# Kernel tuning notes

Hardware: AMD Instinct MI355X
Metric: run time of the kernel (lower is better)

Reference implementation:

```python
import jax, jax.numpy as jnp
import numpy as np

N, E = 100000, 800000
IN, HID, H, C, L, OUT = 32, 128, 4, 32, 3, 5
NEG_SLOPE = 0.2
EPS = 1e-5


def setup_inputs() -> dict:
    key = jax.random.key(0)
    ks = jax.random.split(key, 20)
    s = 0.1
    inp = {
        "x": jax.random.normal(ks[0], (N, IN), jnp.float32),
        "edge_index": jax.random.randint(ks[1], (2, E), 0, N, jnp.int64),
        "edge_attr": jax.random.uniform(ks[2], (E, 1), jnp.float32),
        "Win": jax.random.normal(ks[3], (IN, HID), jnp.float32) * s,
        "b_in": jnp.zeros((HID,), jnp.float32),
        "Wg": jax.random.normal(ks[4], (L, HID, H * C), jnp.float32) * s,
        "bg": jnp.zeros((L, H * C), jnp.float32),
        "a_src": jax.random.normal(ks[5], (L, H, C), jnp.float32) * s,
        "a_dst": jax.random.normal(ks[6], (L, H, C), jnp.float32) * s,
        "We": jax.random.normal(ks[7], (L, 1, H * C), jnp.float32) * s,
        "a_edge": jax.random.normal(ks[8], (L, H, C), jnp.float32) * s,
        "ln_w": jnp.ones((L, HID), jnp.float32),
        "ln_b": jnp.zeros((L, HID), jnp.float32),
        "Wout": jax.random.normal(ks[9], (HID, OUT), jnp.float32) * s,
        "bout": jnp.zeros((OUT,), jnp.float32),
    }
    return inp


def _add_self_loops(src, dst, ea):
    # PyG fill_value='mean': self-loop attr = mean of incoming edge attrs per node
    ones = jnp.ones((src.shape[0],), ea.dtype)
    deg = jax.ops.segment_sum(ones, dst, N)
    loop_attr = jax.ops.segment_sum(ea, dst, N) / jnp.maximum(deg, 1.0)[:, None]
    idx = jnp.arange(N, dtype=src.dtype)
    return (jnp.concatenate([src, idx]), jnp.concatenate([dst, idx]),
            jnp.concatenate([ea, loop_attr], axis=0))


def _gat_conv(x, src, dst, ea, Wg, bg, a_s, a_d, We, a_e):
    xh = (x @ Wg).reshape(N, H, C)                    # [N,H,C]
    al_s = jnp.einsum('nhc,hc->nh', xh, a_s)          # [N,H]
    al_d = jnp.einsum('nhc,hc->nh', xh, a_d)
    ee = (ea @ We).reshape(-1, H, C)                  # [Et,H,C]
    al_e = jnp.einsum('ehc,hc->eh', ee, a_e)
    logits = jax.nn.leaky_relu(al_s[src] + al_d[dst] + al_e, NEG_SLOPE)
    m = jax.ops.segment_max(logits, dst, N)
    m = jnp.where(jnp.isfinite(m), m, 0.0)
    ex = jnp.exp(logits - m[dst])
    den = jax.ops.segment_sum(ex, dst, N)
    alpha = ex / (den[dst] + 1e-16)                   # segment softmax over dst
    out = jax.ops.segment_sum(alpha[:, :, None] * xh[src], dst, N)
    return out.reshape(N, H * C) + bg


def _graph_layernorm(h, w, b):
    # PyG LayerNorm(mode='graph'): normalize over all nodes and features
    h = h - jnp.mean(h)
    var = jnp.mean(h * h)
    return h / jnp.sqrt(var + EPS) * w + b


def reference(x, edge_index, edge_attr, Win, b_in, Wg, bg, a_src, a_dst, We,
              a_edge, ln_w, ln_b, Wout, bout):
    src, dst = edge_index[0], edge_index[1]
    src, dst, ea = _add_self_loops(src, dst, edge_attr)
    h = x @ Win + b_in
    for l in range(L):
        g = _gat_conv(h, src, dst, ea, Wg[l], bg[l], a_src[l], a_dst[l],
                      We[l], a_edge[l])
        g = _graph_layernorm(g, ln_w[l], ln_b[l])
        h = jax.nn.relu(g + h)
    return h @ Wout + bout
```

## Files before the change

### kernel.cpp

```cpp
#include <hip/hip_runtime.h>
#include <hip/hip_bf16.h>

#define NN 100000
#define EE 800000
#define HID 128
#define NH 4
#define CH 32
#define NL 3
#define NOUT 5
#define NEG_SLOPE 0.2f
#define LN_EPS 1e-5f
#define GCAP 64
#define NB_SCAN 98
#define HQ (HID / 2)
#define WB_LSZ 9216
#define HB4 782
#define SB4 782
#define NG64 1563

typedef unsigned int u32;
typedef __attribute__((ext_vector_type(8))) short bf16x8;
typedef __attribute__((ext_vector_type(4))) float f32x4;

static __device__ __forceinline__ float bflo(u32 r) { return __uint_as_float(r << 16); }
static __device__ __forceinline__ float bfhi(u32 r) { return __uint_as_float(r & 0xffff0000u); }
static __device__ __forceinline__ unsigned short f2bf(float x) {
    union U { __hip_bfloat16 b; unsigned short s; } u;
    u.b = __float2bfloat16(x);
    return u.s;
}
static __device__ __forceinline__ u32 pack2(float a, float b) {
    return (u32)f2bf(a) | ((u32)f2bf(b) << 16);
}
static __device__ __forceinline__ float lrelu(float x) {
    return x > 0.f ? x : NEG_SLOPE * x;
}

__global__ void hist_prep_kernel(const int* __restrict__ ei, int* __restrict__ cnt,
                                 u32* __restrict__ slot,
                                 const float* __restrict__ We, const float* __restrict__ a_e,
                                 float* __restrict__ wedot,
                                 const float* __restrict__ Win, const float* __restrict__ b_in,
                                 const float* __restrict__ Wg, float* __restrict__ wf,
                                 const float* __restrict__ a_src, const float* __restrict__ a_dst,
                                 u32* __restrict__ wb, float* __restrict__ wga) {
    int b = blockIdx.x, t = threadIdx.x;
    if (b < HB4) {
        int e0 = b * 1024 + t;
        #pragma unroll
        for (int k = 0; k < 4; k++) {
            int e = e0 + k * 256;
            if (e < EE) {
                int d = ei[EE + e];
                int s = atomicAdd(&cnt[d], 1);
                slot[e] = ((u32)d << 8) | (u32)s;
            }
        }
        return;
    }
    if (b == HB4) {
        if (t < NL * NH) {
            int l = t >> 2, hh = t & 3;
            float s = 0.f;
            #pragma unroll
            for (int c = 0; c < CH; c++)
                s += We[l * HID + hh * CH + c] * a_e[l * HID + hh * CH + c];
            wedot[t] = s;
        }
        for (int i = t; i < HID * 8; i += 256) {
            int m = i >> 3, j = i & 7;
            int hh = j & 3;
            const float* a = (j < 4) ? (a_src + hh * CH) : (a_dst + hh * CH);
            const float* wrow = Wg + (size_t)m * HID + hh * CH;
            float s = 0.f;
            #pragma unroll
            for (int c = 0; c < CH; c++) s += wrow[c] * a[c];
            wga[i] = s;
        }
        return;
    }
    if (b < HB4 + 18) {
        int idx = (b - HB4 - 1) * 256 + t;
        if (idx >= 33 * HID) return;
        int r = idx >> 7, c = idx & 127;
        float acc = 0.f;
        for (int k = 0; k < HID; k++) {
            float a = (r < 32) ? Win[r * HID + k] : b_in[k];
            acc += a * Wg[(size_t)k * HID + c];
        }
        wf[r * HID + c] = acc;
        return;
    }
    {
        int idx = (b - HB4 - 18) * 256 + t;
        if (idx >= 2 * 2304) return;
        int l = idx / 2304;
        int rem = idx % 2304;
        int ks = rem / 576;
        int ct = (rem % 576) / 64;
        int lane = rem % 64;
        int q = lane >> 4, n = lane & 15;
        const float* W = Wg + (size_t)(l + 1) * HID * HID;
        float v[8];
        if (ct < 8) {
            #pragma unroll
            for (int j = 0; j < 8; j++) {
                int k = ks * 32 + q * 8 + j;
                v[j] = W[(size_t)k * HID + ct * 16 + n];
            }
        } else {
            #pragma unroll
            for (int j = 0; j < 8; j++) v[j] = 0.f;
            if (n < 8) {
                const float* a = (n < 4) ? (a_src + (l + 1) * HID + (n & 3) * CH)
                                         : (a_dst + (l + 1) * HID + (n & 3) * CH);
                #pragma unroll
                for (int j = 0; j < 8; j++) {
                    int k = ks * 32 + q * 8 + j;
                    const float* wrow = W + (size_t)k * HID + (n & 3) * CH;
                    float s = 0.f;
                    for (int c = 0; c < CH; c++) s += wrow[c] * a[c];
                    v[j] = s;
                }
            }
        }
        u32* dst = wb + (size_t)l * WB_LSZ + (size_t)((ks * 9 + ct) * 64 + lane) * 4;
        dst[0] = pack2(v[0], v[1]); dst[1] = pack2(v[2], v[3]);
        dst[2] = pack2(v[4], v[5]); dst[3] = pack2(v[6], v[7]);
    }
}

__global__ __launch_bounds__(1024) void scan_prep2_kernel(const int* __restrict__ cnt,
        int* __restrict__ rowptr, int* __restrict__ sums, int* __restrict__ prefixes,
        int* __restrict__ flags,
        const float* __restrict__ Win, const float* __restrict__ b_in,
        const float* __restrict__ wga, float* __restrict__ wf, u32* __restrict__ wb2) {
    if (blockIdx.x >= NB_SCAN) {
        int b = blockIdx.x - NB_SCAN;
        int lane = threadIdx.x;
        if (lane >= 64) return;
        int q = lane >> 4, n = lane & 15;
        if (b == 17) {
            if (lane < 8) {
                float s = 0.f;
                for (int m = 0; m < HID; m++) s += b_in[m] * wga[m * 8 + lane];
                wf[33 * HID + lane] = s;
            }
            return;
        }
        float v[8];
        if (b < 8) {
            #pragma unroll
            for (int j = 0; j < 8; j++) v[j] = Win[(q * 8 + j) * HID + b * 16 + n];
        } else if (b < 16) {
            int ct = b - 8;
            #pragma unroll
            for (int j = 0; j < 8; j++) v[j] = wf[(q * 8 + j) * HID + ct * 16 + n];
        } else {
            #pragma unroll
            for (int j = 0; j < 8; j++) v[j] = 0.f;
            if (n < 8) {
                #pragma unroll
                for (int j = 0; j < 8; j++) {
                    const float* wrow = Win + (q * 8 + j) * HID;
                    float s = 0.f;
                    for (int m = 0; m < HID; m++) s += wrow[m] * wga[m * 8 + n];
                    v[j] = s;
                }
            }
        }
        u32* dst = wb2 + (size_t)(b * 64 + lane) * 4;
        dst[0] = pack2(v[0], v[1]); dst[1] = pack2(v[2], v[3]);
        dst[2] = pack2(v[4], v[5]); dst[3] = pack2(v[6], v[7]);
        return;
    }
    __shared__ int ws[16];
    __shared__ int bprefix;
    int b = blockIdx.x;
    int gid = b * 1024 + threadIdx.x;
    int v = (gid < NN) ? cnt[gid] : 0;
    int lane = threadIdx.x & 63, wid = threadIdx.x >> 6;
    int s = v;
    #pragma unroll
    for (int off = 1; off < 64; off <<= 1) {
        int t2 = __shfl_up(s, off, 64);
        if (lane >= off) s += t2;
    }
    if (lane == 63) ws[wid] = s;
    __syncthreads();
    int add = 0;
    for (int w2 = 0; w2 < wid; w2++) add += ws[w2];
    int incl = s + add;
    if (threadIdx.x == 0) {
        int total = 0;
        for (int w2 = 0; w2 < 16; w2++) total += ws[w2];
        atomicExch(&sums[b], total);
        __threadfence();
        atomicExch(&flags[b], 1);
        int pfx = 0;
        for (int i = b - 1; i >= 0; i--) {
            int f;
            do { f = atomicAdd(&flags[i], 0); } while (f == 0);
            if (f == 2) { pfx += atomicAdd(&prefixes[i], 0); break; }
            pfx += atomicAdd(&sums[i], 0);
        }
        atomicExch(&prefixes[b], pfx + total);
        __threadfence();
        atomicExch(&flags[b], 2);
        bprefix = pfx;
    }
    __syncthreads();
    int pfx = bprefix;
    if (gid <= NN) rowptr[gid] = pfx + incl - v;
}

__global__ __launch_bounds__(256) void scatter_ingemm_kernel(
        const int* __restrict__ ei, const float* __restrict__ ea,
        const int* __restrict__ rowptr, const u32* __restrict__ slot,
        uint2* __restrict__ edges,
        const float* __restrict__ x, const u32* __restrict__ wb2,
        const float* __restrict__ wf, const float* __restrict__ b_in,
        u32* __restrict__ h, u32* __restrict__ xh,
        float* __restrict__ al_s, float* __restrict__ al_d) {
    __shared__ u32 xsu[1024];
    if (blockIdx.x < SB4) {
        int e0 = blockIdx.x * 1024 + threadIdx.x;
        #pragma unroll
        for (int k = 0; k < 4; k++) {
            int e = e0 + k * 256;
            if (e < EE) {
                u32 p = slot[e];
                int d = (int)(p >> 8);
                int pos = rowptr[d] + (int)(p & 255u);
                edges[pos] = make_uint2((u32)ei[e], __float_as_uint(ea[e]));
            }
        }
        return;
    }
    int t = threadIdx.x;
    int wv = t >> 6, lane = t & 63;
    int q = lane >> 4, n16 = lane & 15;
    int n0 = (blockIdx.x - SB4) * 64;
    {
        int row = t >> 2, qq = t & 3;
        int gr = n0 + row;
        int rt = row >> 4, m = row & 15;
        uint4 op = make_uint4(0u, 0u, 0u, 0u);
        if (gr < NN) {
            float4 vA = *(const float4*)&x[(size_t)gr * 32 + qq * 8];
            float4 vB = *(const float4*)&x[(size_t)gr * 32 + qq * 8 + 4];
            op.x = pack2(vA.x, vA.y); op.y = pack2(vA.z, vA.w);
            op.z = pack2(vB.x, vB.y); op.w = pack2(vB.z, vB.w);
        }
        *(uint4*)&xsu[(rt * 64 + qq * 16 + m) * 4] = op;
    }
    bf16x8 bwin[2], bwf[2], bal;
    #pragma unroll
    for (int cc = 0; cc < 2; cc++) {
        uint4 r0 = *(const uint4*)&wb2[(size_t)(((wv * 2 + cc)) * 64 + lane) * 4];
        uint4 r1 = *(const uint4*)&wb2[(size_t)((8 + wv * 2 + cc) * 64 + lane) * 4];
        bwin[cc] = __builtin_bit_cast(bf16x8, r0);
        bwf[cc]  = __builtin_bit_cast(bf16x8, r1);
    }
    {
        uint4 r = *(const uint4*)&wb2[(size_t)(16 * 64 + lane) * 4];
        bal = __builtin_bit_cast(bf16x8, r);
    }
    __syncthreads();
    f32x4 acch[4][2], accx[4][2], accal[4];
    #pragma unroll
    for (int rt = 0; rt < 4; rt++) {
        acch[rt][0] = (f32x4){0.f, 0.f, 0.f, 0.f};
        acch[rt][1] = (f32x4){0.f, 0.f, 0.f, 0.f};
        accx[rt][0] = (f32x4){0.f, 0.f, 0.f, 0.f};
        accx[rt][1] = (f32x4){0.f, 0.f, 0.f, 0.f};
        accal[rt]   = (f32x4){0.f, 0.f, 0.f, 0.f};
    }
    #pragma unroll
    for (int rt = 0; rt < 4; rt++) {
        uint4 araw = *(const uint4*)&xsu[(rt * 64 + lane) * 4];
        bf16x8 af = __builtin_bit_cast(bf16x8, araw);
        acch[rt][0] = __builtin_amdgcn_mfma_f32_16x16x32_bf16(af, bwin[0], acch[rt][0], 0, 0, 0);
        acch[rt][1] = __builtin_amdgcn_mfma_f32_16x16x32_bf16(af, bwin[1], acch[rt][1], 0, 0, 0);
        accx[rt][0] = __builtin_amdgcn_mfma_f32_16x16x32_bf16(af, bwf[0], accx[rt][0], 0, 0, 0);
        accx[rt][1] = __builtin_amdgcn_mfma_f32_16x16x32_bf16(af, bwf[1], accx[rt][1], 0, 0, 0);
        if (wv == 3)
            accal[rt] = __builtin_amdgcn_mfma_f32_16x16x32_bf16(af, bal, accal[rt], 0, 0, 0);
    }
    float bi[2], bfv[2];
    #pragma unroll
    for (int cc = 0; cc < 2; cc++) {
        int col = (wv * 2 + cc) * 16 + n16;
        bi[cc] = b_in[col];
        bfv[cc] = wf[32 * HID + col];
    }
    float bfa = (wv == 3 && n16 < 8) ? wf[33 * HID + n16] : 0.f;
    #pragma unroll
    for (int rt = 0; rt < 4; rt++) {
        #pragma unroll
        for (int reg = 0; reg < 4; reg++) {
            int row = n0 + rt * 16 + q * 4 + reg;
            #pragma unroll
            for (int cc = 0; cc < 2; cc++) {
                float v = acch[rt][cc][reg] + bi[cc];
                float vp = __shfl_xor(v, 1, 64);
                float u = accx[rt][cc][reg] + bfv[cc];
                float up = __shfl_xor(u, 1, 64);
                if (!(n16 & 1) && row < NN) {
                    int colp = (wv * 2 + cc) * 8 + (n16 >> 1);
                    h[(size_t)row * HQ + colp] = pack2(v, vp);
                    xh[(size_t)row * HQ + colp] = pack2(u, up);
                }
            }
            if (wv == 3 && row < NN && n16 < 8) {
                float v = accal[rt][reg] + bfa;
                if (n16 < 4) al_s[row * 4 + n16] = v;
                else         al_d[row * 4 + (n16 - 4)] = v;
            }
        }
    }
}

__global__ __launch_bounds__(256) void gemm_mfma_kernel(const u32* __restrict__ h,
        const u32* __restrict__ wb, u32* __restrict__ xh, const u32* __restrict__ g,
        const float* __restrict__ lnw, const float* __restrict__ lnb,
        const float* __restrict__ partials, u32* __restrict__ hout,
        float* __restrict__ al_s, float* __restrict__ al_d) {
    __shared__ u32 hsu[4096];
    __shared__ float sred[8];
    int n0 = blockIdx.x * 64;
    int t = threadIdx.x;
    int wv = t >> 6, lane = t & 63;
    int q = lane >> 4, n16 = lane & 15;

    {
        const float4* pp = (const float4*)partials;
        float4 v0 = pp[t * 2], v1 = pp[t * 2 + 1];
        float s = v0.x + v0.z + v1.x + v1.z;
        float qq = v0.y + v0.w + v1.y + v1.w;
        #pragma unroll
        for (int off = 1; off <= 32; off <<= 1) {
            s += __shfl_xor(s, off, 64);
            qq += __shfl_xor(qq, off, 64);
        }
        if (lane == 0) { sred[wv * 2] = s; sred[wv * 2 + 1] = qq; }
    }
    __syncthreads();
    float S = sred[0] + sred[2] + sred[4] + sred[6];
    float Q = sred[1] + sred[3] + sred[5] + sred[7];
    const float M = (float)NN * (float)HID;
    float mean = S / M;
    float rstd = rsqrtf(fmaxf(Q / M - mean * mean, 0.f) + LN_EPS);

    bf16x8 bfrag[2][4];
    #pragma unroll
    for (int ks = 0; ks < 4; ks++) {
        #pragma unroll
        for (int cc = 0; cc < 2; cc++) {
            int ct = wv * 2 + cc;
            uint4 r = *(const uint4*)&wb[(size_t)((ks * 9 + ct) * 64 + lane) * 4];
            bfrag[cc][ks] = __builtin_bit_cast(bf16x8, r);
        }
    }
    bf16x8 bal[4];
    #pragma unroll
    for (int ks = 0; ks < 4; ks++) {
        uint4 r = *(const uint4*)&wb[(size_t)((ks * 9 + 8) * 64 + lane) * 4];
        bal[ks] = __builtin_bit_cast(bf16x8, r);
    }

    {
        int row = t >> 2;
        int qq = t & 3;
        int gr = n0 + row;
        int rt = row >> 4, m = row & 15;
        #pragma unroll
        for (int ks = 0; ks < 4; ks++) {
            int kk = ks * 32 + qq * 8;
            uint4 op = make_uint4(0u, 0u, 0u, 0u);
            if (gr < NN) {
                size_t base = (size_t)gr * HQ + (kk >> 1);
                uint4 gp = *(const uint4*)&g[base];
                uint4 hp = *(const uint4*)&h[base];
                float4 wA = *(const float4*)&lnw[kk];
                float4 wB = *(const float4*)&lnw[kk + 4];
                float4 bA = *(const float4*)&lnb[kk];
                float4 bB = *(const float4*)&lnb[kk + 4];
                float v0 = fmaxf((bflo(gp.x) - mean) * rstd * wA.x + bA.x + bflo(hp.x), 0.f);
                float v1 = fmaxf((bfhi(gp.x) - mean) * rstd * wA.y + bA.y + bfhi(hp.x), 0.f);
                float v2 = fmaxf((bflo(gp.y) - mean) * rstd * wA.z + bA.z + bflo(hp.y), 0.f);
                float v3 = fmaxf((bfhi(gp.y) - mean) * rstd * wA.w + bA.w + bfhi(hp.y), 0.f);
                float v4 = fmaxf((bflo(gp.z) - mean) * rstd * wB.x + bB.x + bflo(hp.z), 0.f);
                float v5 = fmaxf((bfhi(gp.z) - mean) * rstd * wB.y + bB.y + bfhi(hp.z), 0.f);
                float v6 = fmaxf((bflo(gp.w) - mean) * rstd * wB.z + bB.z + bflo(hp.w), 0.f);
                float v7 = fmaxf((bfhi(gp.w) - mean) * rstd * wB.w + bB.w + bfhi(hp.w), 0.f);
                op.x = pack2(v0, v1); op.y = pack2(v2, v3);
                op.z = pack2(v4, v5); op.w = pack2(v6, v7);
                *(uint4*)&hout[base] = op;
            }
            *(uint4*)&hsu[((rt * 4 + ks) * 64 + qq * 16 + m) * 4] = op;
        }
    }
    __syncthreads();

    f32x4 acc[4][2];
    f32x4 accal[4];
    #pragma unroll
    for (int rt = 0; rt < 4; rt++) {
        acc[rt][0] = (f32x4){0.f, 0.f, 0.f, 0.f};
        acc[rt][1] = (f32x4){0.f, 0.f, 0.f, 0.f};
        accal[rt]  = (f32x4){0.f, 0.f, 0.f, 0.f};
    }
    #pragma unroll
    for (int rt = 0; rt < 4; rt++) {
        #pragma unroll
        for (int ks = 0; ks < 4; ks++) {
            uint4 araw = *(const uint4*)&hsu[((rt * 4 + ks) * 64 + lane) * 4];
            bf16x8 af = __builtin_bit_cast(bf16x8, araw);
            acc[rt][0] = __builtin_amdgcn_mfma_f32_16x16x32_bf16(af, bfrag[0][ks], acc[rt][0], 0, 0, 0);
            acc[rt][1] = __builtin_amdgcn_mfma_f32_16x16x32_bf16(af, bfrag[1][ks], acc[rt][1], 0, 0, 0);
            if (wv == 3)
                accal[rt] = __builtin_amdgcn_mfma_f32_16x16x32_bf16(af, bal[ks], accal[rt], 0, 0, 0);
        }
    }

    #pragma unroll
    for (int rt = 0; rt < 4; rt++) {
        #pragma unroll
        for (int reg = 0; reg < 4; reg++) {
            int row = n0 + rt * 16 + q * 4 + reg;
            #pragma unroll
            for (int cc = 0; cc < 2; cc++) {
                float v = acc[rt][cc][reg];
                float vp = __shfl_xor(v, 1, 64);
                if (!(n16 & 1) && row < NN) {
                    int colp = (wv * 2 + cc) * 8 + (n16 >> 1);
                    xh[(size_t)row * HQ + colp] = pack2(v, vp);
                }
            }
            if (wv == 3 && row < NN && n16 < 8) {
                float v = accal[rt][reg];
                if (n16 < 4) al_s[row * 4 + n16] = v;
                else         al_d[row * 4 + (n16 - 4)] = v;
            }
        }
    }
}

__global__ __launch_bounds__(256) void gat_agg_kernel(const int* __restrict__ rowptr,
        const uint2* __restrict__ edges, const u32* __restrict__ xh,
        const float* __restrict__ al_s, const float* __restrict__ al_d,
        const float* __restrict__ wedot, const float* __restrict__ bg,
        u32* __restrict__ g, float* __restrict__ partials) {
    __shared__ float lds_ex[4][GCAP * 4];
    __shared__ float lds_ea[4][GCAP];
    __shared__ int lds_src[4][GCAP];
    int wv = threadIdx.x >> 6, lane = threadIdx.x & 63;
    int base = (blockIdx.x * 4 + wv) * 4;
    if (base >= NN) return;
    float* ex_w = lds_ex[wv];
    float* ea_w = lds_ea[wv];
    int* src_w = lds_src[wv];
    int b1 = base + 1 < NN ? base + 1 : NN;
    int b2 = base + 2 < NN ? base + 2 : NN;
    int b3 = base + 3 < NN ? base + 3 : NN;
    int b4 = base + 4 < NN ? base + 4 : NN;
    int r0 = rowptr[base], r1 = rowptr[b1], r2 = rowptr[b2], r3 = rowptr[b3], r4 = rowptr[b4];
    int span = r4 - r0;
    int ncached = span < GCAP ? span : GCAP;
    float wd0 = wedot[0], wd1 = wedot[1], wd2 = wedot[2], wd3 = wedot[3];

    for (int i = lane; i < ncached; i += 64) {
        int gi = r0 + i;
        uint2 e = edges[gi];
        int s = (int)e.x;
        float eav = __uint_as_float(e.y);
        int d = (gi >= r1) + (gi >= r2) + (gi >= r3);
        float4 aldv = *(const float4*)&al_d[(base + d) * 4];
        float4 als = *(const float4*)&al_s[s * 4];
        float e0 = __expf(lrelu(als.x + aldv.x + eav * wd0));
        float e1 = __expf(lrelu(als.y + aldv.y + eav * wd1));
        float e2 = __expf(lrelu(als.z + aldv.z + eav * wd2));
        float e3 = __expf(lrelu(als.w + aldv.w + eav * wd3));
        src_w[i] = s;
        ea_w[i] = eav;
        *(float4*)&ex_w[i * 4] = make_float4(e0, e1, e2, e3);
    }

    int nl = lane >> 4, cg = lane & 15;
    int n = base + nl;
    bool nvalid = n < NN;
    int ls = (nl == 0 ? r0 : nl == 1 ? r1 : nl == 2 ? r2 : r3) - r0;
    int le = (nl == 0 ? r1 : nl == 1 ? r2 : nl == 2 ? r3 : r4) - r0;
    int lec = le < ncached ? le : ncached;
    int head = cg >> 2;
    int c4 = cg * 4;
    float wdh = head == 0 ? wd0 : head == 1 ? wd1 : head == 2 ? wd2 : wd3;
    float a0 = 0.f, a1 = 0.f, a2 = 0.f, a3 = 0.f;
    float a4 = 0.f, a5 = 0.f, a6 = 0.f, a7 = 0.f, den = 0.f, easum = 0.f;
    int j = ls;
    for (; j + 3 < lec; j += 4) {
        int s0 = src_w[j], s1 = src_w[j + 1], s2 = src_w[j + 2], s3 = src_w[j + 3];
        float e0 = ex_w[j * 4 + head],       e1 = ex_w[(j + 1) * 4 + head];
        float e2 = ex_w[(j + 2) * 4 + head], e3 = ex_w[(j + 3) * 4 + head];
        uint4 x0 = *(const uint4*)&xh[(size_t)s0 * HQ + c4];
        uint4 x1 = *(const uint4*)&xh[(size_t)s1 * HQ + c4];
        uint4 x2 = *(const uint4*)&xh[(size_t)s2 * HQ + c4];
        uint4 x3 = *(const uint4*)&xh[(size_t)s3 * HQ + c4];
        den += e0 + e1 + e2 + e3;
        easum += ea_w[j] + ea_w[j + 1] + ea_w[j + 2] + ea_w[j + 3];
        a0 += e0 * bflo(x0.x); a1 += e0 * bfhi(x0.x);
        a2 += e0 * bflo(x0.y); a3 += e0 * bfhi(x0.y);
        a4 += e0 * bflo(x0.z); a5 += e0 * bfhi(x0.z);
        a6 += e0 * bflo(x0.w); a7 += e0 * bfhi(x0.w);
        a0 += e1 * bflo(x1.x); a1 += e1 * bfhi(x1.x);
        a2 += e1 * bflo(x1.y); a3 += e1 * bfhi(x1.y);
        a4 += e1 * bflo(x1.z); a5 += e1 * bfhi(x1.z);
        a6 += e1 * bflo(x1.w); a7 += e1 * bfhi(x1.w);
        a0 += e2 * bflo(x2.x); a1 += e2 * bfhi(x2.x);
        a2 += e2 * bflo(x2.y); a3 += e2 * bfhi(x2.y);
        a4 += e2 * bflo(x2.z); a5 += e2 * bfhi(x2.z);
        a6 += e2 * bflo(x2.w); a7 += e2 * bfhi(x2.w);
        a0 += e3 * bflo(x3.x); a1 += e3 * bfhi(x3.x);
        a2 += e3 * bflo(x3.y); a3 += e3 * bfhi(x3.y);
        a4 += e3 * bflo(x3.z); a5 += e3 * bfhi(x3.z);
        a6 += e3 * bflo(x3.w); a7 += e3 * bfhi(x3.w);
    }
    for (; j < lec; j++) {
        int s0 = src_w[j];
        float e0 = ex_w[j * 4 + head];
        uint4 x0 = *(const uint4*)&xh[(size_t)s0 * HQ + c4];
        den += e0;
        easum += ea_w[j];
        a0 += e0 * bflo(x0.x); a1 += e0 * bfhi(x0.x);
        a2 += e0 * bflo(x0.y); a3 += e0 * bfhi(x0.y);
        a4 += e0 * bflo(x0.z); a5 += e0 * bfhi(x0.z);
        a6 += e0 * bflo(x0.w); a7 += e0 * bfhi(x0.w);
    }
    if (le > lec && nvalid) {
        float aldh = al_d[n * 4 + head];
        for (int jt = (ls > lec ? ls : lec); jt < le; jt++) {
            uint2 e = edges[r0 + jt];
            int s = (int)e.x;
            float eav = __uint_as_float(e.y);
            float ex = __expf(lrelu(al_s[s * 4 + head] + aldh + eav * wdh));
            den += ex;
            easum += eav;
            uint4 x0 = *(const uint4*)&xh[(size_t)s * HQ + c4];
            a0 += ex * bflo(x0.x); a1 += ex * bfhi(x0.x);
            a2 += ex * bflo(x0.y); a3 += ex * bfhi(x0.y);
            a4 += ex * bflo(x0.z); a5 += ex * bfhi(x0.z);
            a6 += ex * bflo(x0.w); a7 += ex * bfhi(x0.w);
        }
    }
    if (nvalid) {
        float mea = easum / fmaxf((float)(le - ls), 1.0f);
        float alh = al_s[n * 4 + head] + al_d[n * 4 + head];
        float ex = __expf(lrelu(alh + mea * wdh));
        den += ex;
        uint4 x0 = *(const uint4*)&xh[(size_t)n * HQ + c4];
        a0 += ex * bflo(x0.x); a1 += ex * bfhi(x0.x);
        a2 += ex * bflo(x0.y); a3 += ex * bfhi(x0.y);
        a4 += ex * bflo(x0.z); a5 += ex * bfhi(x0.z);
        a6 += ex * bflo(x0.w); a7 += ex * bfhi(x0.w);
    }

    float inv = 1.0f / (den + 1e-16f);
    int c0 = cg * 8;
    float4 bgA = *(const float4*)&bg[c0];
    float4 bgB = *(const float4*)&bg[c0 + 4];
    float o0 = a0 * inv + bgA.x, o1 = a1 * inv + bgA.y;
    float o2 = a2 * inv + bgA.z, o3 = a3 * inv + bgA.w;
    float o4 = a4 * inv + bgB.x, o5 = a5 * inv + bgB.y;
    float o6 = a6 * inv + bgB.z, o7 = a7 * inv + bgB.w;
    float ss = 0.f, sq = 0.f;
    if (nvalid) {
        uint4 op;
        op.x = pack2(o0, o1); op.y = pack2(o2, o3);
        op.z = pack2(o4, o5); op.w = pack2(o6, o7);
        *(uint4*)&g[(size_t)n * HQ + c4] = op;
        ss = o0 + o1 + o2 + o3 + o4 + o5 + o6 + o7;
        sq = o0 * o0 + o1 * o1 + o2 * o2 + o3 * o3
           + o4 * o4 + o5 * o5 + o6 * o6 + o7 * o7;
    }
    #pragma unroll
    for (int off = 1; off <= 32; off <<= 1) {
        ss += __shfl_xor(ss, off, 64);
        sq += __shfl_xor(sq, off, 64);
    }
    if (lane == 0) {
        int sl = ((blockIdx.x * 4 + wv) & 1023) * 2;
        atomicAdd(&partials[sl], ss);
        atomicAdd(&partials[sl + 1], sq);
    }
}

__global__ __launch_bounds__(256) void ln_out_kernel(const u32* __restrict__ g,
        const u32* __restrict__ h, const float* __restrict__ lnw,
        const float* __restrict__ lnb, const float* __restrict__ partials,
        const float* __restrict__ Wout, const float* __restrict__ bout,
        float* __restrict__ out) {
    __shared__ float wsh[HID * NOUT];
    __shared__ float sred[8];
    int t = threadIdx.x;
    int wv = t >> 6, lane = t & 63;
    {
        const float4* pp = (const float4*)partials;
        float4 v0 = pp[t * 2], v1 = pp[t * 2 + 1];
        float s = v0.x + v0.z + v1.x + v1.z;
        float qq = v0.y + v0.w + v1.y + v1.w;
        #pragma unroll
        for (int off = 1; off <= 32; off <<= 1) {
            s += __shfl_xor(s, off, 64);
            qq += __shfl_xor(qq, off, 64);
        }
        if (lane == 0) { sred[wv * 2] = s; sred[wv * 2 + 1] = qq; }
    }
    for (int i = t; i < HID * NOUT; i += 256) wsh[i] = Wout[i];
    __syncthreads();
    float S = sred[0] + sred[2] + sred[4] + sred[6];
    float Q = sred[1] + sred[3] + sred[5] + sred[7];
    const float M = (float)NN * (float)HID;
    float mean = S / M;
    float rstd = rsqrtf(fmaxf(Q / M - mean * mean, 0.f) + LN_EPS);

    int nl = lane >> 4, cg = lane & 15;
    int n = (blockIdx.x * 4 + wv) * 4 + nl;
    bool nvalid = n < NN;
    float p[NOUT] = {};
    if (nvalid) {
        int c0 = cg * 8;
        uint4 gv = *(const uint4*)&g[(size_t)n * HQ + cg * 4];
        uint4 hv = *(const uint4*)&h[(size_t)n * HQ + cg * 4];
        float4 wA = *(const float4*)&lnw[c0], wB = *(const float4*)&lnw[c0 + 4];
        float4 bA = *(const float4*)&lnb[c0], bB = *(const float4*)&lnb[c0 + 4];
        float o[8];
        o[0] = fmaxf((bflo(gv.x) - mean) * rstd * wA.x + bA.x + bflo(hv.x), 0.f);
        o[1] = fmaxf((bfhi(gv.x) - mean) * rstd * wA.y + bA.y + bfhi(hv.x), 0.f);
        o[2] = fmaxf((bflo(gv.y) - mean) * rstd * wA.z + bA.z + bflo(hv.y), 0.f);
        o[3] = fmaxf((bfhi(gv.y) - mean) * rstd * wA.w + bA.w + bfhi(hv.y), 0.f);
        o[4] = fmaxf((bflo(gv.z) - mean) * rstd * wB.x + bB.x + bflo(hv.z), 0.f);
        o[5] = fmaxf((bfhi(gv.z) - mean) * rstd * wB.y + bB.y + bfhi(hv.z), 0.f);
        o[6] = fmaxf((bflo(gv.w) - mean) * rstd * wB.z + bB.z + bflo(hv.w), 0.f);
        o[7] = fmaxf((bfhi(gv.w) - mean) * rstd * wB.w + bB.w + bfhi(hv.w), 0.f);
        #pragma unroll
        for (int jj = 0; jj < NOUT; jj++) {
            float acc = 0.f;
            #pragma unroll
            for (int k = 0; k < 8; k++) acc += o[k] * wsh[(c0 + k) * NOUT + jj];
            p[jj] = acc;
        }
    }
    #pragma unroll
    for (int off = 1; off <= 8; off <<= 1) {
        #pragma unroll
        for (int jj = 0; jj < NOUT; jj++) p[jj] += __shfl_xor(p[jj], off, 64);
    }
    if (cg == 0 && nvalid) {
        #pragma unroll
        for (int jj = 0; jj < NOUT; jj++)
            out[(size_t)n * NOUT + jj] = p[jj] + bout[jj];
    }
}

extern "C" void kernel_launch(void* const* d_in, const int* in_sizes, int n_in,
                              void* d_out, int out_size, void* d_ws, size_t ws_size,
                              hipStream_t stream) {
    const float* x      = (const float*)d_in[0];
    const int*   ei     = (const int*)d_in[1];
    const float* ea     = (const float*)d_in[2];
    const float* Win    = (const float*)d_in[3];
    const float* b_in   = (const float*)d_in[4];
    const float* Wg     = (const float*)d_in[5];
    const float* bg     = (const float*)d_in[6];
    const float* a_src  = (const float*)d_in[7];
    const float* a_dst  = (const float*)d_in[8];
    const float* We     = (const float*)d_in[9];
    const float* a_edge = (const float*)d_in[10];
    const float* ln_w   = (const float*)d_in[11];
    const float* ln_b   = (const float*)d_in[12];
    const float* Wout   = (const float*)d_in[13];
    const float* bout   = (const float*)d_in[14];
    float* out = (float*)d_out;

    char* w = (char*)d_ws;
    size_t off = 0;
    auto alloc = [&](size_t bytes) -> void* {
        void* p = w + off;
        off = (off + bytes + 255) & ~(size_t)255;
        return p;
    };
    int*   cnt      = (int*)alloc(NN * sizeof(int));
    float* partials = (float*)alloc(3 * 2048 * sizeof(float));
    int*   sums     = (int*)alloc(NB_SCAN * sizeof(int));
    int*   prefixes = (int*)alloc(NB_SCAN * sizeof(int));
    int*   flags    = (int*)alloc(NB_SCAN * sizeof(int));
    size_t zero_span = off;
    u32*   slot    = (u32*)alloc((size_t)EE * sizeof(u32));
    int*   rowptr  = (int*)alloc((NN + 1) * sizeof(int));
    uint2* edges   = (uint2*)alloc((size_t)EE * sizeof(uint2));
    u32*   h       = (u32*)alloc((size_t)NN * HQ * sizeof(u32));
    u32*   g       = (u32*)alloc((size_t)NN * HQ * sizeof(u32));
    u32*   xh      = (u32*)alloc((size_t)NN * HQ * sizeof(u32));
    float* al_s    = (float*)alloc((size_t)NN * NH * sizeof(float));
    float* al_d    = (float*)alloc((size_t)NN * NH * sizeof(float));
    float* wedot   = (float*)alloc(16 * sizeof(float));
    float* wf      = (float*)alloc(34 * HID * sizeof(float));
    float* wga     = (float*)alloc(HID * 8 * sizeof(float));
    u32*   wb      = (u32*)alloc((size_t)2 * WB_LSZ * sizeof(u32));
    u32*   wb2     = (u32*)alloc(17 * 64 * 4 * sizeof(u32));
    (void)ws_size; (void)n_in; (void)in_sizes; (void)out_size;

    hipMemsetAsync(d_ws, 0, zero_span, stream);
    hist_prep_kernel<<<HB4 + 36, 256, 0, stream>>>(ei, cnt, slot, We, a_edge, wedot,
                                                   Win, b_in, Wg, wf, a_src, a_dst,
                                                   wb, wga);
    scan_prep2_kernel<<<NB_SCAN + 18, 1024, 0, stream>>>(cnt, rowptr, sums, prefixes,
                                                         flags, Win, b_in, wga, wf, wb2);
    scatter_ingemm_kernel<<<SB4 + NG64, 256, 0, stream>>>(ei, ea, rowptr, slot, edges,
                                                          x, wb2, wf, b_in, h, xh,
                                                          al_s, al_d);
    for (int l = 0; l < NL; l++) {
        if (l > 0) {
            gemm_mfma_kernel<<<NG64, 256, 0, stream>>>(
                h, wb + (size_t)(l - 1) * WB_LSZ, xh, g,
                ln_w + (size_t)(l - 1) * HID, ln_b + (size_t)(l - 1) * HID,
                partials + (size_t)(l - 1) * 2048, h, al_s, al_d);
        }
        gat_agg_kernel<<<(NN + 15) / 16, 256, 0, stream>>>(
            rowptr, edges, xh, al_s, al_d, wedot + l * 4,
            bg + (size_t)l * HID, g, partials + (size_t)l * 2048);
    }

    ln_out_kernel<<<(NN + 15) / 16, 256, 0, stream>>>(g, h, ln_w + (size_t)2 * HID,
                                                      ln_b + (size_t)2 * HID,
                                                      partials + 2 * 2048, Wout, bout, out);
}
```

Baseline: 390.0 us.

## Process eight nodes per wavefront in GAT aggregation with 16 channels per lane

The GAT aggregation kernel now assigns eight destination nodes per wavefront instead of four, with each lane handling 16 channels (two 16-byte loads per neighbor row) rather than 8. It fetches the row pointers with one lane-parallel load plus shuffles and doubles the LDS edge cache to 128 entries. The histogram and scatter phases also process eight edges per thread with half as many blocks. This amortizes per-wave setup and edge-logit computation over more nodes, but it halves the number of waves and raises register pressure from the 16 accumulators, which may reduce occupancy and the memory-level parallelism of the gathers.

```diff
diff --git a/kernel.cpp b/kernel.cpp
--- a/kernel.cpp
+++ b/kernel.cpp
@@ -10,12 +10,12 @@
 #define NOUT 5
 #define NEG_SLOPE 0.2f
 #define LN_EPS 1e-5f
-#define GCAP 64
+#define GCAP 128
 #define NB_SCAN 98
 #define HQ (HID / 2)
 #define WB_LSZ 9216
-#define HB4 782
-#define SB4 782
+#define HB8 391
+#define SB8 391
 #define NG64 1563
 
 typedef unsigned int u32;
@@ -45,10 +45,10 @@
                                  const float* __restrict__ a_src, const float* __restrict__ a_dst,
                                  u32* __restrict__ wb, float* __restrict__ wga) {
     int b = blockIdx.x, t = threadIdx.x;
-    if (b < HB4) {
-        int e0 = b * 1024 + t;
-        #pragma unroll
-        for (int k = 0; k < 4; k++) {
+    if (b < HB8) {
+        int e0 = b * 2048 + t;
+        #pragma unroll
+        for (int k = 0; k < 8; k++) {
             int e = e0 + k * 256;
             if (e < EE) {
                 int d = ei[EE + e];
@@ -58,7 +58,7 @@
         }
         return;
     }
-    if (b == HB4) {
+    if (b == HB8) {
         if (t < NL * NH) {
             int l = t >> 2, hh = t & 3;
             float s = 0.f;
@@ -79,8 +79,8 @@
         }
         return;
     }
-    if (b < HB4 + 18) {
-        int idx = (b - HB4 - 1) * 256 + t;
+    if (b < HB8 + 18) {
+        int idx = (b - HB8 - 1) * 256 + t;
         if (idx >= 33 * HID) return;
         int r = idx >> 7, c = idx & 127;
         float acc = 0.f;
@@ -92,7 +92,7 @@
         return;
     }
     {
-        int idx = (b - HB4 - 18) * 256 + t;
+        int idx = (b - HB8 - 18) * 256 + t;
         if (idx >= 2 * 2304) return;
         int l = idx / 2304;
         int rem = idx % 2304;
@@ -223,10 +223,10 @@
         u32* __restrict__ h, u32* __restrict__ xh,
         float* __restrict__ al_s, float* __restrict__ al_d) {
     __shared__ u32 xsu[1024];
-    if (blockIdx.x < SB4) {
-        int e0 = blockIdx.x * 1024 + threadIdx.x;
-        #pragma unroll
-        for (int k = 0; k < 4; k++) {
+    if (blockIdx.x < SB8) {
+        int e0 = blockIdx.x * 2048 + threadIdx.x;
+        #pragma unroll
+        for (int k = 0; k < 8; k++) {
             int e = e0 + k * 256;
             if (e < EE) {
                 u32 p = slot[e];
@@ -240,7 +240,7 @@
     int t = threadIdx.x;
     int wv = t >> 6, lane = t & 63;
     int q = lane >> 4, n16 = lane & 15;
-    int n0 = (blockIdx.x - SB4) * 64;
+    int n0 = (blockIdx.x - SB8) * 64;
     {
         int row = t >> 2, qq = t & 3;
         int gr = n0 + row;
@@ -456,17 +456,20 @@
     __shared__ float lds_ea[4][GCAP];
     __shared__ int lds_src[4][GCAP];
     int wv = threadIdx.x >> 6, lane = threadIdx.x & 63;
-    int base = (blockIdx.x * 4 + wv) * 4;
+    int base = (blockIdx.x * 4 + wv) * 8;
     if (base >= NN) return;
     float* ex_w = lds_ex[wv];
     float* ea_w = lds_ea[wv];
     int* src_w = lds_src[wv];
-    int b1 = base + 1 < NN ? base + 1 : NN;
-    int b2 = base + 2 < NN ? base + 2 : NN;
-    int b3 = base + 3 < NN ? base + 3 : NN;
-    int b4 = base + 4 < NN ? base + 4 : NN;
-    int r0 = rowptr[base], r1 = rowptr[b1], r2 = rowptr[b2], r3 = rowptr[b3], r4 = rowptr[b4];
-    int span = r4 - r0;
+    int rv = 0;
+    if (lane < 9) {
+        int idx = base + lane;
+        rv = rowptr[idx < NN ? idx : NN];
+    }
+    int r0 = __shfl(rv, 0, 64), r1 = __shfl(rv, 1, 64), r2 = __shfl(rv, 2, 64);
+    int r3 = __shfl(rv, 3, 64), r4 = __shfl(rv, 4, 64), r5 = __shfl(rv, 5, 64);
+    int r6 = __shfl(rv, 6, 64), r7 = __shfl(rv, 7, 64), r8 = __shfl(rv, 8, 64);
+    int span = r8 - r0;
     int ncached = span < GCAP ? span : GCAP;
     float wd0 = wedot[0], wd1 = wedot[1], wd2 = wedot[2], wd3 = wedot[3];
 
@@ -475,7 +478,8 @@
         uint2 e = edges[gi];
         int s = (int)e.x;
         float eav = __uint_as_float(e.y);
-        int d = (gi >= r1) + (gi >= r2) + (gi >= r3);
+        int d = (gi >= r1) + (gi >= r2) + (gi >= r3) + (gi >= r4)
+              + (gi >= r5) + (gi >= r6) + (gi >= r7);
         float4 aldv = *(const float4*)&al_d[(base + d) * 4];
         float4 als = *(const float4*)&al_s[s * 4];
         float e0 = __expf(lrelu(als.x + aldv.x + eav * wd0));
@@ -487,101 +491,137 @@
         *(float4*)&ex_w[i * 4] = make_float4(e0, e1, e2, e3);
     }
 
-    int nl = lane >> 4, cg = lane & 15;
+    int nl = lane >> 3, cg = lane & 7;
     int n = base + nl;
     bool nvalid = n < NN;
-    int ls = (nl == 0 ? r0 : nl == 1 ? r1 : nl == 2 ? r2 : r3) - r0;
-    int le = (nl == 0 ? r1 : nl == 1 ? r2 : nl == 2 ? r3 : r4) - r0;
-    int lec = le < ncached ? le : ncached;
-    int head = cg >> 2;
-    int c4 = cg * 4;
+    int lsv, lev;
+    {
+        int ra = nl == 0 ? r0 : nl == 1 ? r1 : nl == 2 ? r2 : nl == 3 ? r3
+               : nl == 4 ? r4 : nl == 5 ? r5 : nl == 6 ? r6 : r7;
+        int rb = nl == 0 ? r1 : nl == 1 ? r2 : nl == 2 ? r3 : nl == 3 ? r4
+               : nl == 4 ? r5 : nl == 5 ? r6 : nl == 6 ? r7 : r8;
+        lsv = ra - r0; lev = rb - r0;
+    }
+    int lec = lev < ncached ? lev : ncached;
+    int head = cg >> 1;
+    int c8 = cg * 8;
     float wdh = head == 0 ? wd0 : head == 1 ? wd1 : head == 2 ? wd2 : wd3;
     float a0 = 0.f, a1 = 0.f, a2 = 0.f, a3 = 0.f;
-    float a4 = 0.f, a5 = 0.f, a6 = 0.f, a7 = 0.f, den = 0.f, easum = 0.f;
-    int j = ls;
-    for (; j + 3 < lec; j += 4) {
-        int s0 = src_w[j], s1 = src_w[j + 1], s2 = src_w[j + 2], s3 = src_w[j + 3];
-        float e0 = ex_w[j * 4 + head],       e1 = ex_w[(j + 1) * 4 + head];
-        float e2 = ex_w[(j + 2) * 4 + head], e3 = ex_w[(j + 3) * 4 + head];
-        uint4 x0 = *(const uint4*)&xh[(size_t)s0 * HQ + c4];
-        uint4 x1 = *(const uint4*)&xh[(size_t)s1 * HQ + c4];
-        uint4 x2 = *(const uint4*)&xh[(size_t)s2 * HQ + c4];
-        uint4 x3 = *(const uint4*)&xh[(size_t)s3 * HQ + c4];
-        den += e0 + e1 + e2 + e3;
-        easum += ea_w[j] + ea_w[j + 1] + ea_w[j + 2] + ea_w[j + 3];
-        a0 += e0 * bflo(x0.x); a1 += e0 * bfhi(x0.x);
-        a2 += e0 * bflo(x0.y); a3 += e0 * bfhi(x0.y);
-        a4 += e0 * bflo(x0.z); a5 += e0 * bfhi(x0.z);
-        a6 += e0 * bflo(x0.w); a7 += e0 * bfhi(x0.w);
-        a0 += e1 * bflo(x1.x); a1 += e1 * bfhi(x1.x);
-        a2 += e1 * bflo(x1.y); a3 += e1 * bfhi(x1.y);
-        a4 += e1 * bflo(x1.z); a5 += e1 * bfhi(x1.z);
-        a6 += e1 * bflo(x1.w); a7 += e1 * bfhi(x1.w);
-        a0 += e2 * bflo(x2.x); a1 += e2 * bfhi(x2.x);
-        a2 += e2 * bflo(x2.y); a3 += e2 * bfhi(x2.y);
-        a4 += e2 * bflo(x2.z); a5 += e2 * bfhi(x2.z);
-        a6 += e2 * bflo(x2.w); a7 += e2 * bfhi(x2.w);
-        a0 += e3 * bflo(x3.x); a1 += e3 * bfhi(x3.x);
-        a2 += e3 * bflo(x3.y); a3 += e3 * bfhi(x3.y);
-        a4 += e3 * bflo(x3.z); a5 += e3 * bfhi(x3.z);
-        a6 += e3 * bflo(x3.w); a7 += e3 * bfhi(x3.w);
-    }
-    for (; j < lec; j++) {
+    float a4 = 0.f, a5 = 0.f, a6 = 0.f, a7 = 0.f;
+    float a8 = 0.f, a9 = 0.f, aA = 0.f, aB = 0.f;
+    float aC = 0.f, aD = 0.f, aE = 0.f, aF = 0.f;
+    float den = 0.f, easum = 0.f;
+    int j = lsv;
+    for (; j + 1 < lec; j += 2) {
+        int s0 = src_w[j], s1 = src_w[j + 1];
+        float e0 = ex_w[j * 4 + head], e1 = ex_w[(j + 1) * 4 + head];
+        const u32* p0 = &xh[(size_t)s0 * HQ + c8];
+        const u32* p1 = &xh[(size_t)s1 * HQ + c8];
+        uint4 x0a = *(const uint4*)p0, x0b = *(const uint4*)(p0 + 4);
+        uint4 x1a = *(const uint4*)p1, x1b = *(const uint4*)(p1 + 4);
+        den += e0 + e1;
+        easum += ea_w[j] + ea_w[j + 1];
+        a0 += e0 * bflo(x0a.x); a1 += e0 * bfhi(x0a.x);
+        a2 += e0 * bflo(x0a.y); a3 += e0 * bfhi(x0a.y);
+        a4 += e0 * bflo(x0a.z); a5 += e0 * bfhi(x0a.z);
+        a6 += e0 * bflo(x0a.w); a7 += e0 * bfhi(x0a.w);
+        a8 += e0 * bflo(x0b.x); a9 += e0 * bfhi(x0b.x);
+        aA += e0 * bflo(x0b.y); aB += e0 * bfhi(x0b.y);
+        aC += e0 * bflo(x0b.z); aD += e0 * bfhi(x0b.z);
+        aE += e0 * bflo(x0b.w); aF += e0 * bfhi(x0b.w);
+        a0 += e1 * bflo(x1a.x); a1 += e1 * bfhi(x1a.x);
+        a2 += e1 * bflo(x1a.y); a3 += e1 * bfhi(x1a.y);
+        a4 += e1 * bflo(x1a.z); a5 += e1 * bfhi(x1a.z);
+        a6 += e1 * bflo(x1a.w); a7 += e1 * bfhi(x1a.w);
+        a8 += e1 * bflo(x1b.x); a9 += e1 * bfhi(x1b.x);
+        aA += e1 * bflo(x1b.y); aB += e1 * bfhi(x1b.y);
+        aC += e1 * bflo(x1b.z); aD += e1 * bfhi(x1b.z);
+        aE += e1 * bflo(x1b.w); aF += e1 * bfhi(x1b.w);
+    }
+    if (j < lec) {
         int s0 = src_w[j];
         float e0 = ex_w[j * 4 + head];
-        uint4 x0 = *(const uint4*)&xh[(size_t)s0 * HQ + c4];
+        const u32* p0 = &xh[(size_t)s0 * HQ + c8];
+        uint4 x0a = *(const uint4*)p0, x0b = *(const uint4*)(p0 + 4);
         den += e0;
         easum += ea_w[j];
-        a0 += e0 * bflo(x0.x); a1 += e0 * bfhi(x0.x);
-        a2 += e0 * bflo(x0.y); a3 += e0 * bfhi(x0.y);
-        a4 += e0 * bflo(x0.z); a5 += e0 * bfhi(x0.z);
-        a6 += e0 * bflo(x0.w); a7 += e0 * bfhi(x0.w);
-    }
-    if (le > lec && nvalid) {
+        a0 += e0 * bflo(x0a.x); a1 += e0 * bfhi(x0a.x);
+        a2 += e0 * bflo(x0a.y); a3 += e0 * bfhi(x0a.y);
+        a4 += e0 * bflo(x0a.z); a5 += e0 * bfhi(x0a.z);
+        a6 += e0 * bflo(x0a.w); a7 += e0 * bfhi(x0a.w);
+        a8 += e0 * bflo(x0b.x); a9 += e0 * bfhi(x0b.x);
+        aA += e0 * bflo(x0b.y); aB += e0 * bfhi(x0b.y);
+        aC += e0 * bflo(x0b.z); aD += e0 * bfhi(x0b.z);
+        aE += e0 * bflo(x0b.w); aF += e0 * bfhi(x0b.w);
+        j++;
+    }
+    if (lev > lec && nvalid) {
         float aldh = al_d[n * 4 + head];
-        for (int jt = (ls > lec ? ls : lec); jt < le; jt++) {
+        for (int jt = (lsv > lec ? lsv : lec); jt < lev; jt++) {
             uint2 e = edges[r0 + jt];
             int s = (int)e.x;
             float eav = __uint_as_float(e.y);
             float ex = __expf(lrelu(al_s[s * 4 + head] + aldh + eav * wdh));
             den += ex;
             easum += eav;
-            uint4 x0 = *(const uint4*)&xh[(size_t)s * HQ + c4];
-            a0 += ex * bflo(x0.x); a1 += ex * bfhi(x0.x);
-            a2 += ex * bflo(x0.y); a3 += ex * bfhi(x0.y);
-            a4 += ex * bflo(x0.z); a5 += ex * bfhi(x0.z);
-            a6 += ex * bflo(x0.w); a7 += ex * bfhi(x0.w);
+            const u32* p0 = &xh[(size_t)s * HQ + c8];
+            uint4 x0a = *(const uint4*)p0, x0b = *(const uint4*)(p0 + 4);
+            a0 += ex * bflo(x0a.x); a1 += ex * bfhi(x0a.x);
+            a2 += ex * bflo(x0a.y); a3 += ex * bfhi(x0a.y);
+            a4 += ex * bflo(x0a.z); a5 += ex * bfhi(x0a.z);
+            a6 += ex * bflo(x0a.w); a7 += ex * bfhi(x0a.w);
+            a8 += ex * bflo(x0b.x); a9 += ex * bfhi(x0b.x);
+            aA += ex * bflo(x0b.y); aB += ex * bfhi(x0b.y);
+            aC += ex * bflo(x0b.z); aD += ex * bfhi(x0b.z);
+            aE += ex * bflo(x0b.w); aF += ex * bfhi(x0b.w);
         }
     }
     if (nvalid) {
-        float mea = easum / fmaxf((float)(le - ls), 1.0f);
+        float mea = easum / fmaxf((float)(lev - lsv), 1.0f);
         float alh = al_s[n * 4 + head] + al_d[n * 4 + head];
         float ex = __expf(lrelu(alh + mea * wdh));
         den += ex;
-        uint4 x0 = *(const uint4*)&xh[(size_t)n * HQ + c4];
-        a0 += ex * bflo(x0.x); a1 += ex * bfhi(x0.x);
-        a2 += ex * bflo(x0.y); a3 += ex * bfhi(x0.y);
-        a4 += ex * bflo(x0.z); a5 += ex * bfhi(x0.z);
-        a6 += ex * bflo(x0.w); a7 += ex * bfhi(x0.w);
+        const u32* p0 = &xh[(size_t)n * HQ + c8];
+        uint4 x0a = *(const uint4*)p0, x0b = *(const uint4*)(p0 + 4);
+        a0 += ex * bflo(x0a.x); a1 += ex * bfhi(x0a.x);
+        a2 += ex * bflo(x0a.y); a3 += ex * bfhi(x0a.y);
+        a4 += ex * bflo(x0a.z); a5 += ex * bfhi(x0a.z);
+        a6 += ex * bflo(x0a.w); a7 += ex * bfhi(x0a.w);
+        a8 += ex * bflo(x0b.x); a9 += ex * bfhi(x0b.x);
+        aA += ex * bflo(x0b.y); aB += ex * bfhi(x0b.y);
+        aC += ex * bflo(x0b.z); aD += ex * bfhi(x0b.z);
+        aE += ex * bflo(x0b.w); aF += ex * bfhi(x0b.w);
     }
 
     float inv = 1.0f / (den + 1e-16f);
-    int c0 = cg * 8;
-    float4 bgA = *(const float4*)&bg[c0];
-    float4 bgB = *(const float4*)&bg[c0 + 4];
-    float o0 = a0 * inv + bgA.x, o1 = a1 * inv + bgA.y;
-    float o2 = a2 * inv + bgA.z, o3 = a3 * inv + bgA.w;
-    float o4 = a4 * inv + bgB.x, o5 = a5 * inv + bgB.y;
-    float o6 = a6 * inv + bgB.z, o7 = a7 * inv + bgB.w;
+    int c0 = cg * 16;
+    float4 bg0 = *(const float4*)&bg[c0];
+    float4 bg1 = *(const float4*)&bg[c0 + 4];
+    float4 bg2 = *(const float4*)&bg[c0 + 8];
+    float4 bg3 = *(const float4*)&bg[c0 + 12];
+    float o0 = a0 * inv + bg0.x, o1 = a1 * inv + bg0.y;
+    float o2 = a2 * inv + bg0.z, o3 = a3 * inv + bg0.w;
+    float o4 = a4 * inv + bg1.x, o5 = a5 * inv + bg1.y;
+    float o6 = a6 * inv + bg1.z, o7 = a7 * inv + bg1.w;
+    float o8 = a8 * inv + bg2.x, o9 = a9 * inv + bg2.y;
+    float oA = aA * inv + bg2.z, oB = aB * inv + bg2.w;
+    float oC = aC * inv + bg3.x, oD = aD * inv + bg3.y;
+    float oE = aE * inv + bg3.z, oF = aF * inv + bg3.w;
     float ss = 0.f, sq = 0.f;
     if (nvalid) {
-        uint4 op;
-        op.x = pack2(o0, o1); op.y = pack2(o2, o3);
-        op.z = pack2(o4, o5); op.w = pack2(o6, o7);
-        *(uint4*)&g[(size_t)n * HQ + c4] = op;
-        ss = o0 + o1 + o2 + o3 + o4 + o5 + o6 + o7;
+        uint4 opA, opB;
+        opA.x = pack2(o0, o1); opA.y = pack2(o2, o3);
+        opA.z = pack2(o4, o5); opA.w = pack2(o6, o7);
+        opB.x = pack2(o8, o9); opB.y = pack2(oA, oB);
+        opB.z = pack2(oC, oD); opB.w = pack2(oE, oF);
+        *(uint4*)&g[(size_t)n * HQ + c8] = opA;
+        *(uint4*)&g[(size_t)n * HQ + c8 + 4] = opB;
+        ss = o0 + o1 + o2 + o3 + o4 + o5 + o6 + o7
+           + o8 + o9 + oA + oB + oC + oD + oE + oF;
         sq = o0 * o0 + o1 * o1 + o2 * o2 + o3 * o3
-           + o4 * o4 + o5 * o5 + o6 * o6 + o7 * o7;
+           + o4 * o4 + o5 * o5 + o6 * o6 + o7 * o7
+           + o8 * o8 + o9 * o9 + oA * oA + oB * oB
+           + oC * oC + oD * oD + oE * oE + oF * oF;
     }
     #pragma unroll
     for (int off = 1; off <= 32; off <<= 1) {
@@ -712,12 +752,12 @@
     (void)ws_size; (void)n_in; (void)in_sizes; (void)out_size;
 
     hipMemsetAsync(d_ws, 0, zero_span, stream);
-    hist_prep_kernel<<<HB4 + 36, 256, 0, stream>>>(ei, cnt, slot, We, a_edge, wedot,
+    hist_prep_kernel<<<HB8 + 36, 256, 0, stream>>>(ei, cnt, slot, We, a_edge, wedot,
                                                    Win, b_in, Wg, wf, a_src, a_dst,
                                                    wb, wga);
     scan_prep2_kernel<<<NB_SCAN + 18, 1024, 0, stream>>>(cnt, rowptr, sums, prefixes,
                                                          flags, Win, b_in, wga, wf, wb2);
-    scatter_ingemm_kernel<<<SB4 + NG64, 256, 0, stream>>>(ei, ea, rowptr, slot, edges,
+    scatter_ingemm_kernel<<<SB8 + NG64, 256, 0, stream>>>(ei, ea, rowptr, slot, edges,
                                                           x, wb2, wf, b_in, h, xh,
                                                           al_s, al_d);
     for (int l = 0; l < NL; l++) {
@@ -727,7 +767,7 @@
                 ln_w + (size_t)(l - 1) * HID, ln_b + (size_t)(l - 1) * HID,
                 partials + (size_t)(l - 1) * 2048, h, al_s, al_d);
         }
-        gat_agg_kernel<<<(NN + 15) / 16, 256, 0, stream>>>(
+        gat_agg_kernel<<<(NN + 31) / 32, 256, 0, stream>>>(
             rowptr, edges, xh, al_s, al_d, wedot + l * 4,
             bg + (size_t)l * HID, g, partials + (size_t)l * 2048);
     }
```

After: 382.9 us. About the same (-1.8%).
